# Kernel tuning notes

Measured on AMD Instinct MI355X. Metric: run time of the kernel, lower is better.

The kernel has to match this reference:

```python
import jax, jax.numpy as jnp
import numpy as np

N_NODES = 100000   # m for both sparse matmuls (graph adjacency is N x N)
ITERATIONS = 10
ALPHA = 0.1
N_FEATURES = 2000
HIDDEN = 64
N_LABELS = 16
NNZ_FEAT = 5000000
N_EDGES = 3200000


def setup_inputs() -> dict:
    key = jax.random.key(0)
    ks = jax.random.split(key, 10)
    feat_rows = jax.random.randint(ks[0], (NNZ_FEAT,), 0, N_NODES, dtype=jnp.int32)
    feat_cols = jax.random.randint(ks[1], (NNZ_FEAT,), 0, N_FEATURES, dtype=jnp.int32)
    feature_values = jax.random.uniform(ks[2], (NNZ_FEAT,), dtype=jnp.float32)
    edge_rows = jax.random.randint(ks[3], (N_EDGES,), 0, N_NODES, dtype=jnp.int32)
    edge_cols = jax.random.randint(ks[4], (N_EDGES,), 0, N_NODES, dtype=jnp.int32)
    edge_weights = jax.random.uniform(ks[5], (N_EDGES,), dtype=jnp.float32) * (1.0 / 32.0)
    W1 = jax.random.normal(ks[6], (N_FEATURES, HIDDEN), dtype=jnp.float32) * 0.05
    b1 = jax.random.normal(ks[7], (HIDDEN,), dtype=jnp.float32) * 0.05
    W2 = jax.random.normal(ks[8], (HIDDEN, N_LABELS), dtype=jnp.float32) * 0.1
    b2 = jax.random.normal(ks[9], (N_LABELS,), dtype=jnp.float32) * 0.1
    return {"feat_rows": feat_rows, "feat_cols": feat_cols, "feature_values": feature_values,
            "edge_rows": edge_rows, "edge_cols": edge_cols, "edge_weights": edge_weights,
            "W1": W1, "b1": b1, "W2": W2, "b2": b2}


def spmm(rows, cols, vals, matrix, m):
    # sparse [m, k] (COO) @ dense [k, d]: gather rows of dense, scale, scatter-add
    out = matrix[cols] * vals[:, None]          # [nnz, d]
    return jax.ops.segment_sum(out, rows, num_segments=m)


def reference(feat_rows, feat_cols, feature_values, edge_rows, edge_cols,
              edge_weights, W1, b1, W2, b2):
    # layer 1: sparse features [N, F] @ W1 [F, H] + b1  (eval mode: dropout is identity)
    latent1 = spmm(feat_rows, feat_cols, feature_values, W1, N_NODES) + b1  # [N, H]
    latent1 = jax.nn.relu(latent1)
    z = latent1 @ W2 + b2                       # [N, L] local predictions

    def step(p, _):
        new = spmm(edge_rows, edge_cols, edge_weights, p, N_NODES)  # A_hat @ p
        p = (1.0 - ALPHA) * new + ALPHA * z
        return p, None

    preds, _ = jax.lax.scan(step, z, None, length=ITERATIONS)
    return jax.nn.log_softmax(preds, axis=1)
```

## Files before the change

kernel.cpp:

```cpp
#include <hip/hip_runtime.h>

#define N_NODES    100000
#define N_FEATURES 2000
#define HIDDEN     64
#define N_LABELS   16
#define NNZ_FEAT   5000000
#define N_EDGES    3200000
#define ITERS      10
#define ALPHA      0.1f

#define CBSH       9
#define CROWS      (1 << CBSH)
#define NBC        ((N_NODES + CROWS - 1) >> CBSH)
#define TILE       8192
#define NFB        ((NNZ_FEAT + TILE - 1) / TILE)
#define NEB        ((N_EDGES + TILE - 1) / TILE)

#define EQMUL  1048544.0f
#define EWDEC  (0.028125f / 32767.0f)

__device__ __forceinline__ unsigned short f2bf(float x) {
    unsigned u = __float_as_uint(x);
    u += 0x7FFF + ((u >> 16) & 1);
    return (unsigned short)(u >> 16);
}
__device__ __forceinline__ float bf2f(unsigned short h) {
    return __uint_as_float(((unsigned)h) << 16);
}
__device__ __forceinline__ float bf_lo(unsigned u) { return __uint_as_float(u << 16); }
__device__ __forceinline__ float bf_hi(unsigned u) { return __uint_as_float(u & 0xFFFF0000u); }


__global__ __launch_bounds__(256) void zero_int(int* __restrict__ p, int n) {
    int t = blockIdx.x * 256 + threadIdx.x;
    if (t < n) p[t] = 0;
}

__global__ __launch_bounds__(256) void hist2_k(const int* __restrict__ frows, int nf,
                                               int* __restrict__ cbf,
                                               const int* __restrict__ erows, int ne,
                                               int* __restrict__ cbe) {
    __shared__ int h[NBC];
    for (int i = threadIdx.x; i < NBC; i += 256) h[i] = 0;
    __syncthreads();
    const int* rows; int n; int* dst; int b0, nb;
    if (blockIdx.x < 1280) { rows = frows; n = nf; dst = cbf; b0 = blockIdx.x; nb = 1280; }
    else                   { rows = erows; n = ne; dst = cbe; b0 = blockIdx.x - 1280; nb = 768; }
    int stride = nb * 256;
    for (int i = b0 * 256 + threadIdx.x; i < n; i += stride)
        atomicAdd(&h[rows[i] >> CBSH], 1);
    __syncthreads();
    for (int i = threadIdx.x; i < NBC; i += 256)
        if (h[i]) atomicAdd(&dst[i], h[i]);
}

__global__ __launch_bounds__(256) void scan2_k(const int* __restrict__ cbf,
                                               int* __restrict__ cbasef, int* __restrict__ gbf,
                                               int* __restrict__ frp,
                                               const int* __restrict__ cbe,
                                               int* __restrict__ cbasee, int* __restrict__ gbe,
                                               int* __restrict__ erp) {
    const int* cnt; int* cbase; int* gbcur; int* rp;
    if (blockIdx.x == 0) { cnt = cbf; cbase = cbasef; gbcur = gbf; rp = frp; }
    else                 { cnt = cbe; cbase = cbasee; gbcur = gbe; rp = erp; }
    __shared__ int s[256];
    int t = threadIdx.x;
    int v = (t < NBC) ? cnt[t] : 0;
    s[t] = v;
    __syncthreads();
    for (int off = 1; off < 256; off <<= 1) {
        int a = (t >= off) ? s[t - off] : 0;
        __syncthreads();
        s[t] += a;
        __syncthreads();
    }
    if (t < NBC) { cbase[t] = s[t] - v; gbcur[t] = s[t] - v; }
    if (t == NBC - 1) { cbase[NBC] = s[t]; rp[N_NODES] = s[t]; }
}

__global__ __launch_bounds__(1024) void binA2_k(
    const int* __restrict__ frows, const int* __restrict__ fcols, const float* __restrict__ fvals,
    int* __restrict__ gbf, int* __restrict__ fpk, unsigned short* __restrict__ frl,
    const int* __restrict__ erows, const int* __restrict__ ecols, const float* __restrict__ evals,
    int* __restrict__ gbe, int* __restrict__ epk, unsigned short* __restrict__ erl)
{
    __shared__ int            staged_pk[TILE];
    __shared__ unsigned short staged_rl[TILE];
    __shared__ unsigned char  sbkt[TILE];
    __shared__ int cnt[NBC];
    __shared__ int rstart[NBC];
    __shared__ int gbase[NBC];
    __shared__ int sc[256];

    const int* rows; const int* cols; const float* vals;
    int* gbcur; int* bpk; unsigned short* brl;
    int n, qshift, bfval; float qmul;
    int bid = blockIdx.x;
    if (bid < NFB) {
        rows = frows; cols = fcols; vals = fvals; gbcur = gbf; bpk = fpk; brl = frl;
        n = NNZ_FEAT; qshift = 16; qmul = 0.f; bfval = 1;
    } else {
        bid -= NFB;
        rows = erows; cols = ecols; vals = evals; gbcur = gbe; bpk = epk; brl = erl;
        n = N_EDGES; qshift = 17; qmul = EQMUL; bfval = 0;
    }

    int tid = threadIdx.x;
    int base = bid * TILE;
    int m = n - base; if (m > TILE) m = TILE;

    for (int i = tid; i < NBC; i += 1024) cnt[i] = 0;
    __syncthreads();

    int seq[TILE / 1024];
    int rbuf[TILE / 1024];
    #pragma unroll
    for (int k = 0; k < TILE / 1024; ++k) {
        int j = k * 1024 + tid;
        if (j < m) {
            int r = rows[base + j];
            rbuf[k] = r;
            seq[k] = atomicAdd(&cnt[r >> CBSH], 1);
        }
    }
    __syncthreads();

    if (tid < 256) sc[tid] = (tid < NBC) ? cnt[tid] : 0;
    __syncthreads();
    for (int off = 1; off < 256; off <<= 1) {
        int a = 0;
        if (tid < 256 && tid >= off) a = sc[tid - off];
        __syncthreads();
        if (tid < 256) sc[tid] += a;
        __syncthreads();
    }
    if (tid < NBC) rstart[tid] = sc[tid] - cnt[tid];
    __syncthreads();

    #pragma unroll
    for (int k = 0; k < TILE / 1024; ++k) {
        int j = k * 1024 + tid;
        if (j < m) {
            int r = rbuf[k];
            int b = r >> CBSH;
            float v = vals[base + j];
            int q = bfval ? (int)f2bf(v) : __float2int_rn(v * qmul);
            int slot = rstart[b] + seq[k];
            staged_pk[slot] = (q << qshift) | cols[base + j];
            staged_rl[slot] = (unsigned short)(r & (CROWS - 1));
            sbkt[slot] = (unsigned char)b;
        }
    }
    __syncthreads();

    if (tid < NBC && cnt[tid] > 0) gbase[tid] = atomicAdd(&gbcur[tid], cnt[tid]);
    __syncthreads();

    #pragma unroll
    for (int k = 0; k < TILE / 1024; ++k) {
        int slot = k * 1024 + tid;
        if (slot < m) {
            int b = sbkt[slot];
            int dst = gbase[b] + (slot - rstart[b]);
            bpk[dst] = staged_pk[slot];
            brl[dst] = staged_rl[slot];
        }
    }
}

__global__ __launch_bounds__(1024) void binB2x_k(
    const int* __restrict__ fpk, const unsigned short* __restrict__ frl,
    const int* __restrict__ cbasef, int* __restrict__ frp, int* __restrict__ fcw,
    const int* __restrict__ epk, const unsigned short* __restrict__ erl,
    const int* __restrict__ cbasee, int* __restrict__ erp, int* __restrict__ ecw)
{
    const int* bin_pk; const unsigned short* bin_rl; const int* cbase; int* rp; int* cw;
    int b = blockIdx.x;
    if (b < NBC) { bin_pk = fpk; bin_rl = frl; cbase = cbasef; rp = frp; cw = fcw; }
    else { b -= NBC; bin_pk = epk; bin_rl = erl; cbase = cbasee; rp = erp; cw = ecw; }

    int r0 = b << CBSH;
    int nrows = N_NODES - r0; if (nrows > CROWS) nrows = CROWS;
    __shared__ int hist[CROWS];
    __shared__ int sc[CROWS];
    int t = threadIdx.x;
    if (t < CROWS) hist[t] = 0;
    __syncthreads();
    int s = cbase[b], e = cbase[b + 1];
    for (int i = s + t; i < e; i += 1024)
        atomicAdd(&hist[bin_rl[i]], 1);
    __syncthreads();
    if (t < CROWS) sc[t] = hist[t];
    __syncthreads();
    for (int off = 1; off < CROWS; off <<= 1) {
        int a = (t >= off && t < CROWS) ? sc[t - off] : 0;
        __syncthreads();
        if (t < CROWS) sc[t] += a;
        __syncthreads();
    }
    if (t < CROWS) {
        int excl = sc[t] - hist[t] + s;
        if (t < nrows) rp[r0 + t] = excl;
        hist[t] = excl;
    }
    __syncthreads();
    for (int i = s + t; i < e; i += 1024) {
        int pos = atomicAdd(&hist[bin_rl[i]], 1);
        cw[pos] = bin_pk[i];
    }
}


__global__ __launch_bounds__(256) void w1_to_bf16(const float* __restrict__ W1,
                                                  unsigned short* __restrict__ W1b) {
    int t = blockIdx.x * 256 + threadIdx.x;
    if (t < N_FEATURES * HIDDEN / 4) {
        float4 v = reinterpret_cast<const float4*>(W1)[t];
        ushort4 o;
        o.x = f2bf(v.x); o.y = f2bf(v.y); o.z = f2bf(v.z); o.w = f2bf(v.w);
        reinterpret_cast<ushort4*>(W1b)[t] = o;
    }
}

__global__ __launch_bounds__(256) void spmm_fused(const int* __restrict__ rp,
                                                  const int* __restrict__ cwp,
                                                  const unsigned short* __restrict__ W1b,
                                                  const float* __restrict__ b1,
                                                  const float* __restrict__ W2,
                                                  const float* __restrict__ b2,
                                                  float* __restrict__ z,
                                                  unsigned short* __restrict__ pb0) {
    __shared__ float sW2T[N_LABELS * (HIDDEN + 1)];
    __shared__ float sb1[HIDDEN];
    __shared__ float sb2[N_LABELS];
    for (int i = threadIdx.x; i < HIDDEN * N_LABELS; i += 256) {
        int h = i >> 4, l = i & 15;
        sW2T[l * (HIDDEN + 1) + h] = W2[i];
    }
    if (threadIdx.x < HIDDEN) sb1[threadIdx.x] = b1[threadIdx.x];
    if (threadIdx.x < N_LABELS) sb2[threadIdx.x] = b2[threadIdx.x];
    __syncthreads();

    int t = blockIdx.x * 256 + threadIdx.x;
    int row = t >> 3, sl = t & 7;
    if (row >= N_NODES) return;
    int s = rp[row], e = rp[row + 1];
    int hbase = sl * 8;

    float acc[8];
    #pragma unroll
    for (int j = 0; j < 8; ++j) acc[j] = 0.f;

    int i = s;
    for (; i + 3 < e; i += 4) {
        uint4 wv[4]; float vv[4];
        #pragma unroll
        for (int k = 0; k < 4; ++k) {
            int pk = cwp[i + k];
            vv[k] = bf_hi((unsigned)pk);
            wv[k] = *reinterpret_cast<const uint4*>(W1b + (size_t)(pk & 0x7FF) * HIDDEN + hbase);
        }
        #pragma unroll
        for (int k = 0; k < 4; ++k) {
            acc[0] = fmaf(vv[k], bf_lo(wv[k].x), acc[0]);
            acc[1] = fmaf(vv[k], bf_hi(wv[k].x), acc[1]);
            acc[2] = fmaf(vv[k], bf_lo(wv[k].y), acc[2]);
            acc[3] = fmaf(vv[k], bf_hi(wv[k].y), acc[3]);
            acc[4] = fmaf(vv[k], bf_lo(wv[k].z), acc[4]);
            acc[5] = fmaf(vv[k], bf_hi(wv[k].z), acc[5]);
            acc[6] = fmaf(vv[k], bf_lo(wv[k].w), acc[6]);
            acc[7] = fmaf(vv[k], bf_hi(wv[k].w), acc[7]);
        }
    }
    for (; i < e; ++i) {
        int pk = cwp[i];
        float v = bf_hi((unsigned)pk);
        uint4 w = *reinterpret_cast<const uint4*>(W1b + (size_t)(pk & 0x7FF) * HIDDEN + hbase);
        acc[0] = fmaf(v, bf_lo(w.x), acc[0]);
        acc[1] = fmaf(v, bf_hi(w.x), acc[1]);
        acc[2] = fmaf(v, bf_lo(w.y), acc[2]);
        acc[3] = fmaf(v, bf_hi(w.y), acc[3]);
        acc[4] = fmaf(v, bf_lo(w.z), acc[4]);
        acc[5] = fmaf(v, bf_hi(w.z), acc[5]);
        acc[6] = fmaf(v, bf_lo(w.w), acc[6]);
        acc[7] = fmaf(v, bf_hi(w.w), acc[7]);
    }

    float part[16];
    #pragma unroll
    for (int l = 0; l < 16; ++l) part[l] = 0.f;
    #pragma unroll
    for (int j = 0; j < 8; ++j) {
        float a = acc[j] + sb1[hbase + j];
        a = a > 0.f ? a : 0.f;
        #pragma unroll
        for (int l = 0; l < 16; ++l)
            part[l] = fmaf(a, sW2T[l * (HIDDEN + 1) + hbase + j], part[l]);
    }
    #pragma unroll
    for (int l = 0; l < 8; ++l) {
        float lo = __shfl_xor(part[l], 1);
        float hi = __shfl_xor(part[l + 8], 1);
        part[l] = (sl & 1) ? (part[l + 8] + hi) : (part[l] + lo);
    }
    #pragma unroll
    for (int l = 0; l < 4; ++l) {
        float lo = __shfl_xor(part[l], 2);
        float hi = __shfl_xor(part[l + 4], 2);
        part[l] = (sl & 2) ? (part[l + 4] + hi) : (part[l] + lo);
    }
    #pragma unroll
    for (int l = 0; l < 2; ++l) {
        float lo = __shfl_xor(part[l], 4);
        float hi = __shfl_xor(part[l + 2], 4);
        part[l] = (sl & 4) ? (part[l + 2] + hi) : (part[l] + lo);
    }
    int lbase = 8 * (sl & 1) + 4 * ((sl >> 1) & 1) + 2 * ((sl >> 2) & 1);
    float z0 = part[0] + sb2[lbase];
    float z1 = part[1] + sb2[lbase + 1];
    *reinterpret_cast<float2*>(z + (size_t)row * N_LABELS + lbase) = make_float2(z0, z1);
    unsigned o = (unsigned)f2bf(z0) | ((unsigned)f2bf(z1) << 16);
    *reinterpret_cast<unsigned*>(pb0 + (size_t)row * N_LABELS + lbase) = o;
}

__global__ __launch_bounds__(256) void prop_bf16(const int* __restrict__ rp,
                                                 const int* __restrict__ cwp,
                                                 const float* __restrict__ z,
                                                 const unsigned short* __restrict__ pin,
                                                 unsigned short* __restrict__ pout) {
    int t = blockIdx.x * 256 + threadIdx.x;
    int row = t >> 2, sub = t & 3;
    if (row >= N_NODES) return;
    int s = rp[row], e = rp[row + 1];
    float4 zv = *reinterpret_cast<const float4*>(z + (size_t)row * N_LABELS + sub * 4);
    float a0 = ALPHA * zv.x, a1 = ALPHA * zv.y, a2 = ALPHA * zv.z, a3 = ALPHA * zv.w;
    int i = s;
    if ((i & 1) && i < e) {
        int pk = cwp[i];
        float w = (float)((unsigned)pk >> 17) * EWDEC;
        uint2 q = *reinterpret_cast<const uint2*>(pin + (size_t)(pk & 0x1FFFF) * N_LABELS + sub * 4);
        a0 = fmaf(w, bf_lo(q.x), a0); a1 = fmaf(w, bf_hi(q.x), a1);
        a2 = fmaf(w, bf_lo(q.y), a2); a3 = fmaf(w, bf_hi(q.y), a3);
        ++i;
    }
    for (; i + 7 < e; i += 8) {
        int2 cA = *reinterpret_cast<const int2*>(cwp + i);
        int2 cB = *reinterpret_cast<const int2*>(cwp + i + 2);
        int2 cC = *reinterpret_cast<const int2*>(cwp + i + 4);
        int2 cD = *reinterpret_cast<const int2*>(cwp + i + 6);
        int pks[8] = {cA.x, cA.y, cB.x, cB.y, cC.x, cC.y, cD.x, cD.y};
        uint2 q[8]; float w[8];
        #pragma unroll
        for (int k = 0; k < 8; ++k) {
            int pk = pks[k];
            w[k] = (float)((unsigned)pk >> 17) * EWDEC;
            q[k] = *reinterpret_cast<const uint2*>(pin + (size_t)(pk & 0x1FFFF) * N_LABELS + sub * 4);
        }
        #pragma unroll
        for (int k = 0; k < 8; ++k) {
            a0 = fmaf(w[k], bf_lo(q[k].x), a0); a1 = fmaf(w[k], bf_hi(q[k].x), a1);
            a2 = fmaf(w[k], bf_lo(q[k].y), a2); a3 = fmaf(w[k], bf_hi(q[k].y), a3);
        }
    }
    for (; i < e; ++i) {
        int pk = cwp[i];
        float w = (float)((unsigned)pk >> 17) * EWDEC;
        uint2 q = *reinterpret_cast<const uint2*>(pin + (size_t)(pk & 0x1FFFF) * N_LABELS + sub * 4);
        a0 = fmaf(w, bf_lo(q.x), a0); a1 = fmaf(w, bf_hi(q.x), a1);
        a2 = fmaf(w, bf_lo(q.y), a2); a3 = fmaf(w, bf_hi(q.y), a3);
    }
    uint2 o;
    o.x = (unsigned)f2bf(a0) | ((unsigned)f2bf(a1) << 16);
    o.y = (unsigned)f2bf(a2) | ((unsigned)f2bf(a3) << 16);
    *reinterpret_cast<uint2*>(pout + (size_t)row * N_LABELS + sub * 4) = o;
}

__global__ __launch_bounds__(256) void prop_final(const int* __restrict__ rp,
                                                  const int* __restrict__ cwp,
                                                  const float* __restrict__ z,
                                                  const unsigned short* __restrict__ pin,
                                                  float* __restrict__ out) {
    int t = blockIdx.x * 256 + threadIdx.x;
    int row = t >> 2, sub = t & 3;
    if (row >= N_NODES) return;
    int s = rp[row], e = rp[row + 1];
    float4 zv = *reinterpret_cast<const float4*>(z + (size_t)row * N_LABELS + sub * 4);
    float a0 = ALPHA * zv.x, a1 = ALPHA * zv.y, a2 = ALPHA * zv.z, a3 = ALPHA * zv.w;
    int i = s;
    if ((i & 1) && i < e) {
        int pk = cwp[i];
        float w = (float)((unsigned)pk >> 17) * EWDEC;
        uint2 q = *reinterpret_cast<const uint2*>(pin + (size_t)(pk & 0x1FFFF) * N_LABELS + sub * 4);
        a0 = fmaf(w, bf_lo(q.x), a0); a1 = fmaf(w, bf_hi(q.x), a1);
        a2 = fmaf(w, bf_lo(q.y), a2); a3 = fmaf(w, bf_hi(q.y), a3);
        ++i;
    }
    for (; i + 7 < e; i += 8) {
        int2 cA = *reinterpret_cast<const int2*>(cwp + i);
        int2 cB = *reinterpret_cast<const int2*>(cwp + i + 2);
        int2 cC = *reinterpret_cast<const int2*>(cwp + i + 4);
        int2 cD = *reinterpret_cast<const int2*>(cwp + i + 6);
        int pks[8] = {cA.x, cA.y, cB.x, cB.y, cC.x, cC.y, cD.x, cD.y};
        uint2 q[8]; float w[8];
        #pragma unroll
        for (int k = 0; k < 8; ++k) {
            int pk = pks[k];
            w[k] = (float)((unsigned)pk >> 17) * EWDEC;
            q[k] = *reinterpret_cast<const uint2*>(pin + (size_t)(pk & 0x1FFFF) * N_LABELS + sub * 4);
        }
        #pragma unroll
        for (int k = 0; k < 8; ++k) {
            a0 = fmaf(w[k], bf_lo(q[k].x), a0); a1 = fmaf(w[k], bf_hi(q[k].x), a1);
            a2 = fmaf(w[k], bf_lo(q[k].y), a2); a3 = fmaf(w[k], bf_hi(q[k].y), a3);
        }
    }
    for (; i < e; ++i) {
        int pk = cwp[i];
        float w = (float)((unsigned)pk >> 17) * EWDEC;
        uint2 q = *reinterpret_cast<const uint2*>(pin + (size_t)(pk & 0x1FFFF) * N_LABELS + sub * 4);
        a0 = fmaf(w, bf_lo(q.x), a0); a1 = fmaf(w, bf_hi(q.x), a1);
        a2 = fmaf(w, bf_lo(q.y), a2); a3 = fmaf(w, bf_hi(q.y), a3);
    }
    float m = fmaxf(fmaxf(a0, a1), fmaxf(a2, a3));
    m = fmaxf(m, __shfl_xor(m, 1));
    m = fmaxf(m, __shfl_xor(m, 2));
    float ssum = __expf(a0 - m) + __expf(a1 - m) + __expf(a2 - m) + __expf(a3 - m);
    ssum += __shfl_xor(ssum, 1);
    ssum += __shfl_xor(ssum, 2);
    float lse = m + __logf(ssum);
    float4 o = make_float4(a0 - lse, a1 - lse, a2 - lse, a3 - lse);
    *reinterpret_cast<float4*>(out + (size_t)row * N_LABELS + sub * 4) = o;
}


__global__ __launch_bounds__(256) void zero_f4(float4* __restrict__ p, int n4) {
    int t = blockIdx.x * 256 + threadIdx.x;
    if (t < n4) p[t] = make_float4(0.f, 0.f, 0.f, 0.f);
}

__global__ __launch_bounds__(256) void spmm_feat_atomic(
    const int* __restrict__ rows, const int* __restrict__ cols,
    const float* __restrict__ vals, const float* __restrict__ W1,
    float* __restrict__ latent)
{
    long long t = (long long)blockIdx.x * 256 + threadIdx.x;
    if (t >= (long long)NNZ_FEAT * 16) return;
    int e  = (int)(t >> 4);
    int dg = (int)(t & 15);
    int r = rows[e]; int c = cols[e]; float v = vals[e];
    float4 w = *reinterpret_cast<const float4*>(W1 + (size_t)c * HIDDEN + dg * 4);
    float* dst = latent + (size_t)r * HIDDEN + dg * 4;
    atomicAdd(dst + 0, v * w.x); atomicAdd(dst + 1, v * w.y);
    atomicAdd(dst + 2, v * w.z); atomicAdd(dst + 3, v * w.w);
}

__global__ __launch_bounds__(256) void compute_z(const float* __restrict__ latent,
                                                 const float* __restrict__ b1,
                                                 const float* __restrict__ W2,
                                                 const float* __restrict__ b2,
                                                 float* __restrict__ z) {
    __shared__ float sW2[HIDDEN * N_LABELS];
    __shared__ float sb1[HIDDEN];
    for (int i = threadIdx.x; i < HIDDEN * N_LABELS; i += 256) sW2[i] = W2[i];
    if (threadIdx.x < HIDDEN) sb1[threadIdx.x] = b1[threadIdx.x];
    __syncthreads();
    int t = blockIdx.x * 256 + threadIdx.x;
    int node = t >> 4;
    int l = t & 15;
    if (node >= N_NODES) return;
    float acc = b2[l];
    const float* lat = latent + (size_t)node * HIDDEN;
    #pragma unroll 8
    for (int h = 0; h < HIDDEN; ++h) {
        float a = lat[h] + sb1[h];
        a = a > 0.f ? a : 0.f;
        acc = fmaf(a, sW2[h * N_LABELS + l], acc);
    }
    z[(size_t)node * N_LABELS + l] = acc;
}

__global__ __launch_bounds__(256) void init_acc(const float* __restrict__ z,
                                                float* __restrict__ acc) {
    int t = blockIdx.x * 256 + threadIdx.x;
    if (t < N_NODES * N_LABELS / 4) {
        float4 zv = reinterpret_cast<const float4*>(z)[t];
        reinterpret_cast<float4*>(acc)[t] =
            make_float4(ALPHA * zv.x, ALPHA * zv.y, ALPHA * zv.z, ALPHA * zv.w);
    }
}

__global__ __launch_bounds__(256) void edge_scatter(
    const int* __restrict__ rows, const int* __restrict__ cols,
    const float* __restrict__ w, const float* __restrict__ p,
    float* __restrict__ acc)
{
    long long t = (long long)blockIdx.x * 256 + threadIdx.x;
    if (t >= (long long)N_EDGES * 4) return;
    int e = (int)(t >> 2);
    int part = (int)(t & 3);
    int r = rows[e]; int c = cols[e];
    float wt = w[e] * (1.0f - ALPHA);
    float4 pv = *reinterpret_cast<const float4*>(p + (size_t)c * N_LABELS + part * 4);
    float* dst = acc + (size_t)r * N_LABELS + part * 4;
    atomicAdd(dst + 0, wt * pv.x); atomicAdd(dst + 1, wt * pv.y);
    atomicAdd(dst + 2, wt * pv.z); atomicAdd(dst + 3, wt * pv.w);
}

__global__ __launch_bounds__(256) void logsoftmax_k(const float* __restrict__ p,
                                                    float* __restrict__ out) {
    int node = blockIdx.x * 256 + threadIdx.x;
    if (node >= N_NODES) return;
    const float4* src = reinterpret_cast<const float4*>(p + (size_t)node * N_LABELS);
    float4 a = src[0], b = src[1], c = src[2], d = src[3];
    float x[16] = {a.x,a.y,a.z,a.w, b.x,b.y,b.z,b.w, c.x,c.y,c.z,c.w, d.x,d.y,d.z,d.w};
    float m = x[0];
    #pragma unroll
    for (int i = 1; i < 16; ++i) m = fmaxf(m, x[i]);
    float s = 0.f;
    #pragma unroll
    for (int i = 0; i < 16; ++i) s += expf(x[i] - m);
    float lse = m + logf(s);
    float4* o = reinterpret_cast<float4*>(out + (size_t)node * N_LABELS);
    o[0] = make_float4(x[0]-lse,  x[1]-lse,  x[2]-lse,  x[3]-lse);
    o[1] = make_float4(x[4]-lse,  x[5]-lse,  x[6]-lse,  x[7]-lse);
    o[2] = make_float4(x[8]-lse,  x[9]-lse,  x[10]-lse, x[11]-lse);
    o[3] = make_float4(x[12]-lse, x[13]-lse, x[14]-lse, x[15]-lse);
}


extern "C" void kernel_launch(void* const* d_in, const int* in_sizes, int n_in,
                              void* d_out, int out_size, void* d_ws, size_t ws_size,
                              hipStream_t stream)
{
    const int*   feat_rows = (const int*)d_in[0];
    const int*   feat_cols = (const int*)d_in[1];
    const float* feat_vals = (const float*)d_in[2];
    const int*   edge_rows = (const int*)d_in[3];
    const int*   edge_cols = (const int*)d_in[4];
    const float* edge_w    = (const float*)d_in[5];
    const float* W1 = (const float*)d_in[6];
    const float* b1 = (const float*)d_in[7];
    const float* W2 = (const float*)d_in[8];
    const float* b2 = (const float*)d_in[9];
    float* out = (float*)d_out;

    size_t need = 0;
    size_t o_feat_cw = need; need += (size_t)NNZ_FEAT;
    size_t o_edge_cw = need; need += (size_t)N_EDGES;
    size_t o_latent  = need; need += (size_t)N_NODES * HIDDEN;
    size_t o_z       = need; need += (size_t)N_NODES * N_LABELS;
    size_t o_p0      = need; need += (size_t)N_NODES * N_LABELS;
    size_t o_p1      = need; need += (size_t)N_NODES * N_LABELS;
    size_t o_frp     = need; need += N_NODES + 1;
    size_t o_erp     = need; need += N_NODES + 1;
    size_t o_w1b     = need; need += (size_t)N_FEATURES * HIDDEN / 2;
    size_t o_ebin_pk = need; need += (size_t)N_EDGES;
    size_t o_ebin_rl = need; need += (size_t)N_EDGES / 2;
    size_t o_cbf     = need; need += NBC;
    size_t o_cbe     = need; need += NBC;
    size_t o_cbasef  = need; need += NBC + 1;
    size_t o_cbasee  = need; need += NBC + 1;
    size_t o_gbf     = need; need += NBC;
    size_t o_gbe     = need; need += NBC;
    size_t need_bytes = need * 4 + 64;

    float* base = (float*)d_ws;
    float* latent = base + o_latent;
    float* z  = base + o_z;
    float* p0 = base + o_p0;
    float* p1 = base + o_p1;

    if (ws_size >= need_bytes) {
        int* feat_cw = (int*)(base + o_feat_cw);
        int* edge_cw = (int*)(base + o_edge_cw);
        int* feat_rp = (int*)(base + o_frp);
        int* edge_rp = (int*)(base + o_erp);
        unsigned short* W1b = (unsigned short*)(base + o_w1b);
        int* cbf    = (int*)(base + o_cbf);
        int* cbe    = (int*)(base + o_cbe);
        int* cbasef = (int*)(base + o_cbasef);
        int* cbasee = (int*)(base + o_cbasee);
        int* gbf    = (int*)(base + o_gbf);
        int* gbe    = (int*)(base + o_gbe);
        int*            fbin_pk = (int*)(base + o_latent);
        unsigned short* fbin_rl = (unsigned short*)(base + o_z);
        int*            ebin_pk = (int*)(base + o_ebin_pk);
        unsigned short* ebin_rl = (unsigned short*)(base + o_ebin_rl);
        unsigned short* pb0 = (unsigned short*)p0;
        unsigned short* pb1 = (unsigned short*)p1;

        w1_to_bf16<<<(N_FEATURES * HIDDEN / 4 + 255) / 256, 256, 0, stream>>>(W1, W1b);
        zero_int<<<2, 256, 0, stream>>>(cbf, NBC);
        zero_int<<<2, 256, 0, stream>>>(cbe, NBC);
        hist2_k<<<2048, 256, 0, stream>>>(feat_rows, NNZ_FEAT, cbf, edge_rows, N_EDGES, cbe);
        scan2_k<<<2, 256, 0, stream>>>(cbf, cbasef, gbf, feat_rp, cbe, cbasee, gbe, edge_rp);
        binA2_k<<<NFB + NEB, 1024, 0, stream>>>(
            feat_rows, feat_cols, feat_vals, gbf, fbin_pk, fbin_rl,
            edge_rows, edge_cols, edge_w, gbe, ebin_pk, ebin_rl);
        binB2x_k<<<2 * NBC, 1024, 0, stream>>>(
            fbin_pk, fbin_rl, cbasef, feat_rp, feat_cw,
            ebin_pk, ebin_rl, cbasee, edge_rp, edge_cw);

        spmm_fused<<<(N_NODES * 8 + 255) / 256, 256, 0, stream>>>(
            feat_rp, feat_cw, W1b, b1, W2, b2, z, pb0);

        const unsigned short* pin = pb0;
        int pgrid = (N_NODES * 4 + 255) / 256;
        for (int it = 0; it < ITERS - 1; ++it) {
            unsigned short* pout = (it & 1) ? pb0 : pb1;
            prop_bf16<<<pgrid, 256, 0, stream>>>(edge_rp, edge_cw, z, pin, pout);
            pin = pout;
        }
        prop_final<<<pgrid, 256, 0, stream>>>(edge_rp, edge_cw, z, pin, out);
    } else {
        int n4 = N_NODES * HIDDEN / 4;
        zero_f4<<<(n4 + 255) / 256, 256, 0, stream>>>((float4*)latent, n4);
        long long total = (long long)NNZ_FEAT * 16;
        spmm_feat_atomic<<<(int)((total + 255) / 256), 256, 0, stream>>>(
            feat_rows, feat_cols, feat_vals, W1, latent);
        compute_z<<<N_NODES * 16 / 256, 256, 0, stream>>>(latent, b1, W2, b2, z);
        const float* pin = z;
        float* bufs[2] = {p0, p1};
        for (int it = 0; it < ITERS; ++it) {
            float* pout = bufs[it & 1];
            init_acc<<<(N_NODES * N_LABELS / 4 + 255) / 256, 256, 0, stream>>>(z, pout);
            long long tot = (long long)N_EDGES * 4;
            edge_scatter<<<(int)((tot + 255) / 256), 256, 0, stream>>>(
                edge_rows, edge_cols, edge_w, pin, pout);
            pin = pout;
        }
        logsoftmax_k<<<(N_NODES + 255) / 256, 256, 0, stream>>>(pin, out);
    }
}
```

Measured before the change: 519.8 us.

## Stage CSR bin scatter in LDS, store alpha*z as bf16, merge zero launches

The second binning pass now scatters each bucket's packed column/weight entries into a shared-memory staging array and then writes them to global memory contiguously, replacing random global scatter writes. There is a fallback when a bucket exceeds the staging capacity. The z teleport term is stored pre-scaled by alpha in bf16 rather than fp32, which halves its per-iteration read traffic in all propagation kernels. The two zeroing launches are merged into one, which assumes cbf and cbe are adjacent in memory. The large shared array (112 KB) limits occupancy, and bf16 alpha*z adds rounding error.

```diff
diff --git a/kernel.cpp b/kernel.cpp
--- a/kernel.cpp
+++ b/kernel.cpp
@@ -15,6 +15,7 @@
 #define TILE       8192
 #define NFB        ((NNZ_FEAT + TILE - 1) / TILE)
 #define NEB        ((N_EDGES + TILE - 1) / TILE)
+#define BCAP       28672
 
 #define EQMUL  1048544.0f
 #define EWDEC  (0.028125f / 32767.0f)
@@ -168,7 +169,7 @@
     }
 }
 
-__global__ __launch_bounds__(1024) void binB2x_k(
+__global__ __launch_bounds__(1024) void binB3_k(
     const int* __restrict__ fpk, const unsigned short* __restrict__ frl,
     const int* __restrict__ cbasef, int* __restrict__ frp, int* __restrict__ fcw,
     const int* __restrict__ epk, const unsigned short* __restrict__ erl,
@@ -181,12 +182,14 @@
 
     int r0 = b << CBSH;
     int nrows = N_NODES - r0; if (nrows > CROWS) nrows = CROWS;
+    __shared__ int staged[BCAP];
     __shared__ int hist[CROWS];
     __shared__ int sc[CROWS];
     int t = threadIdx.x;
     if (t < CROWS) hist[t] = 0;
     __syncthreads();
     int s = cbase[b], e = cbase[b + 1];
+    int cnt = e - s;
     for (int i = s + t; i < e; i += 1024)
         atomicAdd(&hist[bin_rl[i]], 1);
     __syncthreads();
@@ -199,14 +202,25 @@
         __syncthreads();
     }
     if (t < CROWS) {
-        int excl = sc[t] - hist[t] + s;
-        if (t < nrows) rp[r0 + t] = excl;
+        int excl = sc[t] - hist[t];
+        if (t < nrows) rp[r0 + t] = excl + s;
         hist[t] = excl;
     }
     __syncthreads();
-    for (int i = s + t; i < e; i += 1024) {
-        int pos = atomicAdd(&hist[bin_rl[i]], 1);
-        cw[pos] = bin_pk[i];
+
+    if (cnt <= BCAP) {
+        for (int i = s + t; i < e; i += 1024) {
+            int pos = atomicAdd(&hist[bin_rl[i]], 1);
+            staged[pos] = bin_pk[i];
+        }
+        __syncthreads();
+        for (int j = t; j < cnt; j += 1024)
+            cw[s + j] = staged[j];
+    } else {
+        for (int i = s + t; i < e; i += 1024) {
+            int pos = atomicAdd(&hist[bin_rl[i]], 1);
+            cw[s + pos] = bin_pk[i];
+        }
     }
 }
 
@@ -228,7 +242,7 @@
                                                   const float* __restrict__ b1,
                                                   const float* __restrict__ W2,
                                                   const float* __restrict__ b2,
-                                                  float* __restrict__ z,
+                                                  unsigned short* __restrict__ az,
                                                   unsigned short* __restrict__ pb0) {
     __shared__ float sW2T[N_LABELS * (HIDDEN + 1)];
     __shared__ float sb1[HIDDEN];
@@ -318,22 +332,23 @@
     int lbase = 8 * (sl & 1) + 4 * ((sl >> 1) & 1) + 2 * ((sl >> 2) & 1);
     float z0 = part[0] + sb2[lbase];
     float z1 = part[1] + sb2[lbase + 1];
-    *reinterpret_cast<float2*>(z + (size_t)row * N_LABELS + lbase) = make_float2(z0, z1);
-    unsigned o = (unsigned)f2bf(z0) | ((unsigned)f2bf(z1) << 16);
-    *reinterpret_cast<unsigned*>(pb0 + (size_t)row * N_LABELS + lbase) = o;
+    unsigned oz = (unsigned)f2bf(z0) | ((unsigned)f2bf(z1) << 16);
+    unsigned oa = (unsigned)f2bf(ALPHA * z0) | ((unsigned)f2bf(ALPHA * z1) << 16);
+    *reinterpret_cast<unsigned*>(pb0 + (size_t)row * N_LABELS + lbase) = oz;
+    *reinterpret_cast<unsigned*>(az  + (size_t)row * N_LABELS + lbase) = oa;
 }
 
 __global__ __launch_bounds__(256) void prop_bf16(const int* __restrict__ rp,
                                                  const int* __restrict__ cwp,
-                                                 const float* __restrict__ z,
+                                                 const unsigned short* __restrict__ az,
                                                  const unsigned short* __restrict__ pin,
                                                  unsigned short* __restrict__ pout) {
     int t = blockIdx.x * 256 + threadIdx.x;
     int row = t >> 2, sub = t & 3;
     if (row >= N_NODES) return;
     int s = rp[row], e = rp[row + 1];
-    float4 zv = *reinterpret_cast<const float4*>(z + (size_t)row * N_LABELS + sub * 4);
-    float a0 = ALPHA * zv.x, a1 = ALPHA * zv.y, a2 = ALPHA * zv.z, a3 = ALPHA * zv.w;
+    uint2 azw = *reinterpret_cast<const uint2*>(az + (size_t)row * N_LABELS + sub * 4);
+    float a0 = bf_lo(azw.x), a1 = bf_hi(azw.x), a2 = bf_lo(azw.y), a3 = bf_hi(azw.y);
     int i = s;
     if ((i & 1) && i < e) {
         int pk = cwp[i];
@@ -377,15 +392,15 @@
 
 __global__ __launch_bounds__(256) void prop_final(const int* __restrict__ rp,
                                                   const int* __restrict__ cwp,
-                                                  const float* __restrict__ z,
+                                                  const unsigned short* __restrict__ az,
                                                   const unsigned short* __restrict__ pin,
                                                   float* __restrict__ out) {
     int t = blockIdx.x * 256 + threadIdx.x;
     int row = t >> 2, sub = t & 3;
     if (row >= N_NODES) return;
     int s = rp[row], e = rp[row + 1];
-    float4 zv = *reinterpret_cast<const float4*>(z + (size_t)row * N_LABELS + sub * 4);
-    float a0 = ALPHA * zv.x, a1 = ALPHA * zv.y, a2 = ALPHA * zv.z, a3 = ALPHA * zv.w;
+    uint2 azw = *reinterpret_cast<const uint2*>(az + (size_t)row * N_LABELS + sub * 4);
+    float a0 = bf_lo(azw.x), a1 = bf_hi(azw.x), a2 = bf_lo(azw.y), a3 = bf_hi(azw.y);
     int i = s;
     if ((i & 1) && i < e) {
         int pk = cwp[i];
@@ -586,32 +601,32 @@
         unsigned short* fbin_rl = (unsigned short*)(base + o_z);
         int*            ebin_pk = (int*)(base + o_ebin_pk);
         unsigned short* ebin_rl = (unsigned short*)(base + o_ebin_rl);
+        unsigned short* az  = (unsigned short*)z;
         unsigned short* pb0 = (unsigned short*)p0;
         unsigned short* pb1 = (unsigned short*)p1;
 
         w1_to_bf16<<<(N_FEATURES * HIDDEN / 4 + 255) / 256, 256, 0, stream>>>(W1, W1b);
-        zero_int<<<2, 256, 0, stream>>>(cbf, NBC);
-        zero_int<<<2, 256, 0, stream>>>(cbe, NBC);
+        zero_int<<<2, 256, 0, stream>>>(cbf, 2 * NBC);
         hist2_k<<<2048, 256, 0, stream>>>(feat_rows, NNZ_FEAT, cbf, edge_rows, N_EDGES, cbe);
         scan2_k<<<2, 256, 0, stream>>>(cbf, cbasef, gbf, feat_rp, cbe, cbasee, gbe, edge_rp);
         binA2_k<<<NFB + NEB, 1024, 0, stream>>>(
             feat_rows, feat_cols, feat_vals, gbf, fbin_pk, fbin_rl,
             edge_rows, edge_cols, edge_w, gbe, ebin_pk, ebin_rl);
-        binB2x_k<<<2 * NBC, 1024, 0, stream>>>(
+        binB3_k<<<2 * NBC, 1024, 0, stream>>>(
             fbin_pk, fbin_rl, cbasef, feat_rp, feat_cw,
             ebin_pk, ebin_rl, cbasee, edge_rp, edge_cw);
 
         spmm_fused<<<(N_NODES * 8 + 255) / 256, 256, 0, stream>>>(
-            feat_rp, feat_cw, W1b, b1, W2, b2, z, pb0);
+            feat_rp, feat_cw, W1b, b1, W2, b2, az, pb0);
 
         const unsigned short* pin = pb0;
         int pgrid = (N_NODES * 4 + 255) / 256;
         for (int it = 0; it < ITERS - 1; ++it) {
             unsigned short* pout = (it & 1) ? pb0 : pb1;
-            prop_bf16<<<pgrid, 256, 0, stream>>>(edge_rp, edge_cw, z, pin, pout);
+            prop_bf16<<<pgrid, 256, 0, stream>>>(edge_rp, edge_cw, az, pin, pout);
             pin = pout;
         }
-        prop_final<<<pgrid, 256, 0, stream>>>(edge_rp, edge_cw, z, pin, out);
+        prop_final<<<pgrid, 256, 0, stream>>>(edge_rp, edge_cw, az, pin, out);
     } else {
         int n4 = N_NODES * HIDDEN / 4;
         zero_f4<<<(n4 + 255) / 256, 256, 0, stream>>>((float4*)latent, n4);
```

Result: faster. 489.0 us (-5.9%).
